# Kernel optimization log

Hardware: AMD Instinct MI355X
Metric: run time of the kernel (lower is better)

## Reference

```python
import jax, jax.numpy as jnp
import numpy as np

N_NODES = 100000
N_EDGES = 1600000
N_FEAT = 64
HIDDEN = 64
N_GRAPHS = 64
N_CLASSES = 2


def setup_inputs() -> dict:
    key = jax.random.key(0)
    ks = jax.random.split(key, 12)
    x = jax.random.normal(ks[0], (N_NODES, N_FEAT), dtype=jnp.float32)
    edge_index = jax.random.randint(ks[1], (2, N_EDGES), 0, N_NODES, dtype=jnp.int32)
    batch = jnp.sort(jax.random.randint(ks[2], (N_NODES,), 0, N_GRAPHS, dtype=jnp.int32))
    # Glorot-style init for GCNConv weights, zeros for biases (PyG default)
    def glorot(k, fan_in, fan_out):
        s = jnp.sqrt(6.0 / (fan_in + fan_out))
        return jax.random.uniform(k, (fan_in, fan_out), jnp.float32, -s, s)
    W1 = glorot(ks[3], N_FEAT, HIDDEN); b1 = jnp.zeros((HIDDEN,), jnp.float32)
    W2 = glorot(ks[4], HIDDEN, HIDDEN); b2 = jnp.zeros((HIDDEN,), jnp.float32)
    W3 = glorot(ks[5], HIDDEN, HIDDEN); b3 = jnp.zeros((HIDDEN,), jnp.float32)
    Wl = glorot(ks[6], HIDDEN, N_CLASSES); bl = jnp.zeros((N_CLASSES,), jnp.float32)
    return {"x": x, "edge_index": edge_index, "batch": batch,
            "W1": W1, "b1": b1, "W2": W2, "b2": b2, "W3": W3, "b3": b3,
            "Wl": Wl, "bl": bl}


def _gcn_conv(h, W, b, src, dst, dinv, n_nodes):
    # GCNConv with self-loops: out_i = sum_j d_i^-1/2 d_j^-1/2 (x_j W) + d_i^-1 (x_i W) + b
    h = h @ W                                   # [N, H]
    coef = (dinv[src] * dinv[dst])[:, None]     # [E, 1]
    agg = jax.ops.segment_sum(coef * h[src], dst, num_segments=n_nodes)
    return agg + (dinv * dinv)[:, None] * h + b


def reference(x, edge_index, batch, W1, b1, W2, b2, W3, b3, Wl, bl):
    src, dst = edge_index[0], edge_index[1]
    # degree of A + I (edge weight 1), shared by all three convs
    deg = jax.ops.segment_sum(jnp.ones((N_EDGES,), x.dtype), dst, num_segments=N_NODES) + 1.0
    dinv = jax.lax.rsqrt(deg)

    h = jax.nn.relu(_gcn_conv(x, W1, b1, src, dst, dinv, N_NODES))
    h = jax.nn.relu(_gcn_conv(h, W2, b2, src, dst, dinv, N_NODES))
    h = _gcn_conv(h, W3, b3, src, dst, dinv, N_NODES)

    # global_mean_pool over graph ids
    sums = jax.ops.segment_sum(h, batch, num_segments=N_GRAPHS)
    cnts = jax.ops.segment_sum(jnp.ones((N_NODES,), x.dtype), batch, num_segments=N_GRAPHS)
    pooled = sums / jnp.maximum(cnts, 1.0)[:, None]

    # dropout(p=0.5) is identity in eval mode
    return pooled @ Wl + bl
```

## Files before the change

### kernel.cpp

```cpp
#include <hip/hip_runtime.h>


#define NF 64
#define ELLW 64
#define BINSHIFT 9
#define BINW 512
#define NB 196
#define BINCAP 9216
#define LPITCH 68

typedef __attribute__((ext_vector_type(8))) _Float16 f16x8;
typedef __attribute__((ext_vector_type(4))) _Float16 f16x4;
typedef __attribute__((ext_vector_type(4))) float f32x4;

__device__ inline unsigned short f2h_u(float f) {
    return __builtin_bit_cast(unsigned short, (_Float16)f);
}
__device__ inline unsigned int pack_h2(float a, float b) {
    unsigned int ua = f2h_u(a), ub = f2h_u(b);
    return ua | (ub << 16);
}

__global__ void binA_kernel(const int* __restrict__ src, const int* __restrict__ dst,
                            int* __restrict__ binCnt, int* __restrict__ binEdges,
                            int nE, int chunk) {
    __shared__ int hist[NB];
    __shared__ int base[NB];
    int t = threadIdx.x;
    if (t < NB) hist[t] = 0;
    __syncthreads();
    int e0 = blockIdx.x * chunk;
    int e1 = min(e0 + chunk, nE);
    for (int e = e0 + t; e < e1; e += blockDim.x) {
        int b = dst[e] >> BINSHIFT;
        atomicAdd(&hist[b], 1);
    }
    __syncthreads();
    if (t < NB) {
        base[t] = atomicAdd(&binCnt[t], hist[t]);
        hist[t] = 0;
    }
    __syncthreads();
    for (int e = e0 + t; e < e1; e += blockDim.x) {
        int d = dst[e];
        int b = d >> BINSHIFT;
        int pos = base[b] + atomicAdd(&hist[b], 1);
        if (pos < BINCAP)
            binEdges[(size_t)b * BINCAP + pos] = src[e] | ((d & (BINW - 1)) << 17);
    }
}

__global__ void __launch_bounds__(512) binB_kernel(const int* __restrict__ binEdges,
                            const int* __restrict__ binCnt, int* __restrict__ cnt,
                            float* __restrict__ dinv, int* __restrict__ colELL, int n,
                            unsigned int* __restrict__ dummyA, unsigned int* __restrict__ dummyB) {
    __shared__ int lcnt[BINW];
    int t = threadIdx.x;
    int b = blockIdx.x;
    if (b == 0 && t < 32) { dummyA[t] = 0u; dummyB[t] = 0u; }
    for (int i = t; i < BINW; i += blockDim.x) lcnt[i] = 1;
    __syncthreads();
    int m = binCnt[b];
    if (m > BINCAP) m = BINCAP;
    const int* be = binEdges + (size_t)b * BINCAP;
    int nbase = b << BINSHIFT;
    for (int e = t; e < m; e += blockDim.x) {
        int v = be[e];
        int s = v & 0x1FFFF;
        int dl = v >> 17;
        int pos = atomicAdd(&lcnt[dl], 1);
        if (pos < ELLW) colELL[(size_t)(nbase + dl) * ELLW + pos] = s;
    }
    __syncthreads();
    for (int i = t; i < BINW; i += blockDim.x) {
        int node = nbase + i;
        if (node < n) {
            int c = lcnt[i];
            if (c > ELLW) c = ELLW;
            colELL[(size_t)node * ELLW + 0] = node;
            int cpad = (c + 3) & ~3;
            for (int j = c; j < cpad; ++j)
                colELL[(size_t)node * ELLW + j] = n;
            if (c <= 32) {
                int4 nv; nv.x = n; nv.y = n; nv.z = n; nv.w = n;
                for (int j = cpad; j < 32; j += 4)
                    *(int4*)(colELL + (size_t)node * ELLW + j) = nv;
            }
            cnt[node] = c;
            dinv[node] = rsqrtf((float)c);
        }
    }
}

__global__ void prep_kernel(const float* __restrict__ W1, const float* __restrict__ W2,
                            const float* __restrict__ W3, unsigned short* __restrict__ w1h,
                            unsigned short* __restrict__ w2h, unsigned short* __restrict__ w3h) {
    int t = blockIdx.x * blockDim.x + threadIdx.x;
    if (t < NF * NF) {
        w1h[t] = f2h_u(W1[t]);
        w2h[t] = f2h_u(W2[t]);
        w3h[t] = f2h_u(W3[t]);
    }
}

__device__ __forceinline__ void gather_row32(
        const unsigned short* __restrict__ hB, const int* __restrict__ cr,
        const int* __restrict__ colELL, int row, int c, int es, int fq,
        float& a0, float& a1, float& a2, float& a3) {
    int s0 = cr[0 * 4 + es], s1 = cr[1 * 4 + es];
    int s2 = cr[2 * 4 + es], s3 = cr[3 * 4 + es];
    int s4 = cr[4 * 4 + es], s5 = cr[5 * 4 + es];
    int s6 = cr[6 * 4 + es], s7 = cr[7 * 4 + es];
    f16x4 h0 = __builtin_bit_cast(f16x4, *(const uint2*)(hB + (size_t)s0 * NF + fq * 4));
    f16x4 h1 = __builtin_bit_cast(f16x4, *(const uint2*)(hB + (size_t)s1 * NF + fq * 4));
    f16x4 h2 = __builtin_bit_cast(f16x4, *(const uint2*)(hB + (size_t)s2 * NF + fq * 4));
    f16x4 h3 = __builtin_bit_cast(f16x4, *(const uint2*)(hB + (size_t)s3 * NF + fq * 4));
    f16x4 h4 = __builtin_bit_cast(f16x4, *(const uint2*)(hB + (size_t)s4 * NF + fq * 4));
    f16x4 h5 = __builtin_bit_cast(f16x4, *(const uint2*)(hB + (size_t)s5 * NF + fq * 4));
    f16x4 h6 = __builtin_bit_cast(f16x4, *(const uint2*)(hB + (size_t)s6 * NF + fq * 4));
    f16x4 h7 = __builtin_bit_cast(f16x4, *(const uint2*)(hB + (size_t)s7 * NF + fq * 4));
    f16x4 t0 = (h0 + h1) + (h2 + h3);
    f16x4 t1 = (h4 + h5) + (h6 + h7);
    a0 = (float)t0[0] + (float)t1[0];
    a1 = (float)t0[1] + (float)t1[1];
    a2 = (float)t0[2] + (float)t1[2];
    a3 = (float)t0[3] + (float)t1[3];
    if (c > 32) {
        int nq = (c + 3) >> 2;
        const int* crg = colELL + (size_t)row * ELLW;
        for (int qq = 8; qq < nq; ++qq) {
            int sg = crg[qq * 4 + es];
            f16x4 hg = __builtin_bit_cast(f16x4, *(const uint2*)(hB + (size_t)sg * NF + fq * 4));
            a0 += (float)hg[0]; a1 += (float)hg[1];
            a2 += (float)hg[2]; a3 += (float)hg[3];
        }
    }
}

__device__ inline void load_W_frags(const unsigned short* __restrict__ Wh, int r16, int kq,
                                    f16x8 bfr[4][2]) {
#pragma unroll
    for (int nt = 0; nt < 4; ++nt)
#pragma unroll
        for (int kh = 0; kh < 2; ++kh) {
            f16x8 f;
#pragma unroll
            for (int j = 0; j < 8; ++j)
                f[j] = __builtin_bit_cast(_Float16,
                        Wh[(kh * 32 + kq * 8 + j) * NF + nt * 16 + r16]);
            bfr[nt][kh] = f;
        }
}

__global__ void __launch_bounds__(256) gemm1_mfma_kernel(const float* __restrict__ A,
                                                         const unsigned short* __restrict__ Wh,
                                                         const float* __restrict__ dinv,
                                                         unsigned short* __restrict__ outB, int n) {
    __shared__ unsigned short T[4][16 * LPITCH];
    int lane = threadIdx.x & 63;
    int r16 = lane & 15, kq = lane >> 4;
    int wv = threadIdx.x >> 6;
    int wid = blockIdx.x * 4 + wv;
    int nw = gridDim.x * 4;
    f16x8 bfr[4][2];
    load_W_frags(Wh, r16, kq, bfr);
    int ntiles = n >> 4;
    for (int t = wid; t < ntiles; t += nw) {
        int r0 = t << 4;
        const float* ar = A + (size_t)(r0 + r16) * NF + kq * 8;
        f16x8 a0, a1;
        float4 v0 = *(const float4*)(ar);
        float4 v1 = *(const float4*)(ar + 4);
        float4 v2 = *(const float4*)(ar + 32);
        float4 v3 = *(const float4*)(ar + 36);
        a0[0] = (_Float16)v0.x; a0[1] = (_Float16)v0.y;
        a0[2] = (_Float16)v0.z; a0[3] = (_Float16)v0.w;
        a0[4] = (_Float16)v1.x; a0[5] = (_Float16)v1.y;
        a0[6] = (_Float16)v1.z; a0[7] = (_Float16)v1.w;
        a1[0] = (_Float16)v2.x; a1[1] = (_Float16)v2.y;
        a1[2] = (_Float16)v2.z; a1[3] = (_Float16)v2.w;
        a1[4] = (_Float16)v3.x; a1[5] = (_Float16)v3.y;
        a1[6] = (_Float16)v3.z; a1[7] = (_Float16)v3.w;
        f32x4 acc[4];
#pragma unroll
        for (int nt = 0; nt < 4; ++nt) {
            acc[nt] = (f32x4)(0.0f);
            acc[nt] = __builtin_amdgcn_mfma_f32_16x16x32_f16(a0, bfr[nt][0], acc[nt], 0, 0, 0);
            acc[nt] = __builtin_amdgcn_mfma_f32_16x16x32_f16(a1, bfr[nt][1], acc[nt], 0, 0, 0);
        }
        float ds[4];
#pragma unroll
        for (int reg = 0; reg < 4; ++reg) ds[reg] = dinv[r0 + kq * 4 + reg];
        unsigned short* Tw = T[wv];
#pragma unroll
        for (int nt = 0; nt < 4; ++nt)
#pragma unroll
            for (int reg = 0; reg < 4; ++reg)
                Tw[(kq * 4 + reg) * LPITCH + nt * 16 + r16] = f2h_u(acc[nt][reg] * ds[reg]);
#pragma unroll
        for (int it = 0; it < 4; ++it) {
            int row = it * 4 + kq;
            uint2 v = *(const uint2*)&Tw[row * LPITCH + r16 * 4];
            *(uint2*)(outB + (size_t)(r0 + row) * NF + r16 * 4) = v;
        }
    }
}

__global__ void __launch_bounds__(256) fused_agg_gemm_kernel(
        const unsigned short* __restrict__ hB, const int* __restrict__ colELL,
        const int* __restrict__ cnt, const float* __restrict__ dinv,
        const float* __restrict__ bias, const unsigned short* __restrict__ Wh,
        unsigned short* __restrict__ outB, int n) {
    __shared__ int Icol[16 * 32];
    __shared__ int Icnt[16];
    __shared__ unsigned short Tin[2048];
    __shared__ unsigned short Tout[16 * LPITCH];
    int lane = threadIdx.x & 63;
    int wv = threadIdx.x >> 6;
    int es = lane >> 4, fq = lane & 15;
    int r16 = lane & 15, kq = lane >> 4;
    int r0 = blockIdx.x << 4;
    if (threadIdx.x < 128) {
        int srow = threadIdx.x >> 3, sj = threadIdx.x & 7;
        ((int4*)Icol)[srow * 8 + sj] =
            *(const int4*)(colELL + (size_t)(r0 + srow) * ELLW + sj * 4);
    } else if (threadIdx.x < 144) {
        Icnt[threadIdx.x - 128] = cnt[r0 + threadIdx.x - 128];
    }
    f16x8 bfr0, bfr1;
    {
        f16x8 f0, f1;
#pragma unroll
        for (int j = 0; j < 8; ++j) {
            f0[j] = __builtin_bit_cast(_Float16, Wh[(kq * 8 + j) * NF + wv * 16 + r16]);
            f1[j] = __builtin_bit_cast(_Float16, Wh[(32 + kq * 8 + j) * NF + wv * 16 + r16]);
        }
        bfr0 = f0; bfr1 = f1;
    }
    __syncthreads();
#pragma unroll
    for (int rr = 0; rr < 4; ++rr) {
        int lrow = wv * 4 + rr;
        int row = r0 + lrow;
        int c = Icnt[lrow];
        const int* cr = Icol + lrow * 32;
        float a0, a1, a2, a3;
        gather_row32(hB, cr, colELL, row, c, es, fq, a0, a1, a2, a3);
        a0 += __shfl_xor(a0, 16); a1 += __shfl_xor(a1, 16);
        a2 += __shfl_xor(a2, 16); a3 += __shfl_xor(a3, 16);
        a0 += __shfl_xor(a0, 32); a1 += __shfl_xor(a1, 32);
        a2 += __shfl_xor(a2, 32); a3 += __shfl_xor(a3, 32);
        if (es == 0) {
            float dd = dinv[row];
            float4 b4 = *(const float4*)(bias + fq * 4);
            a0 = fmaxf(dd * a0 + b4.x, 0.f); a1 = fmaxf(dd * a1 + b4.y, 0.f);
            a2 = fmaxf(dd * a2 + b4.z, 0.f); a3 = fmaxf(dd * a3 + b4.w, 0.f);
            uint2 v;
            v.x = pack_h2(a0, a1);
            v.y = pack_h2(a2, a3);
            int ibase = ((fq >> 3) << 10) + (((fq >> 1) & 3) << 7)
                      + (wv * 4 + rr) * 8 + ((fq & 1) << 2);
            *(uint2*)&Tin[ibase] = v;
        }
    }
    __syncthreads();
    f16x8 A0 = *(const f16x8*)&Tin[lane * 8];
    f16x8 A1 = *(const f16x8*)&Tin[1024 + lane * 8];
    f32x4 acc = (f32x4)(0.0f);
    acc = __builtin_amdgcn_mfma_f32_16x16x32_f16(A0, bfr0, acc, 0, 0, 0);
    acc = __builtin_amdgcn_mfma_f32_16x16x32_f16(A1, bfr1, acc, 0, 0, 0);
    float ds[4];
#pragma unroll
    for (int reg = 0; reg < 4; ++reg) ds[reg] = dinv[r0 + kq * 4 + reg];
#pragma unroll
    for (int reg = 0; reg < 4; ++reg)
        Tout[(kq * 4 + reg) * LPITCH + wv * 16 + r16] = f2h_u(acc[reg] * ds[reg]);
    __syncthreads();
    int t = threadIdx.x;
    int orow = t >> 4, ocq = t & 15;
    uint2 v = *(const uint2*)&Tout[orow * LPITCH + ocq * 4];
    *(uint2*)(outB + (size_t)(r0 + orow) * NF + ocq * 4) = v;
}

__global__ void __launch_bounds__(256) gather3_pool_kernel(
        const unsigned short* __restrict__ hB, const int* __restrict__ colELL,
        const int* __restrict__ cnt, const float* __restrict__ dinv,
        const float* __restrict__ bias, const int* __restrict__ batch,
        float* __restrict__ pooled, int n) {
    __shared__ int Icol[16 * 32];
    __shared__ int Icnt[16];
    __shared__ float PL[3][NF];
    int lane = threadIdx.x & 63;
    int wv = threadIdx.x >> 6;
    int es = lane >> 4, fq = lane & 15;
    int ntiles = n >> 4;
    int first = (int)(blockIdx.x << 6);
    if (first > n - 1) first = n - 1;
    int gb = batch[first];
    if (threadIdx.x < 192) PL[threadIdx.x >> 6][threadIdx.x & 63] = 0.f;
    float4 b4 = *(const float4*)(bias + fq * 4);
#pragma unroll 1
    for (int ti = 0; ti < 4; ++ti) {
        int tile = (int)(blockIdx.x << 2) + ti;
        int r0 = tile << 4;
        bool valid = tile < ntiles;
        if (valid) {
            if (threadIdx.x < 128) {
                int srow = threadIdx.x >> 3, sj = threadIdx.x & 7;
                ((int4*)Icol)[srow * 8 + sj] =
                    *(const int4*)(colELL + (size_t)(r0 + srow) * ELLW + sj * 4);
            } else if (threadIdx.x < 144) {
                Icnt[threadIdx.x - 128] = cnt[r0 + threadIdx.x - 128];
            }
        }
        __syncthreads();
        if (valid) {
#pragma unroll
            for (int rr = 0; rr < 4; ++rr) {
                int lrow = wv * 4 + rr;
                int row = r0 + lrow;
                int c = Icnt[lrow];
                const int* cr = Icol + lrow * 32;
                float a0, a1, a2, a3;
                gather_row32(hB, cr, colELL, row, c, es, fq, a0, a1, a2, a3);
                a0 += __shfl_xor(a0, 16); a1 += __shfl_xor(a1, 16);
                a2 += __shfl_xor(a2, 16); a3 += __shfl_xor(a3, 16);
                a0 += __shfl_xor(a0, 32); a1 += __shfl_xor(a1, 32);
                a2 += __shfl_xor(a2, 32); a3 += __shfl_xor(a3, 32);
                if (es == 0) {
                    float dd = dinv[row];
                    float r0f = dd * a0 + b4.x, r1f = dd * a1 + b4.y;
                    float r2f = dd * a2 + b4.z, r3f = dd * a3 + b4.w;
                    int g = batch[row];
                    int sel = g - gb;
                    if (sel < 3) {
                        atomicAdd(&PL[sel][fq * 4 + 0], r0f);
                        atomicAdd(&PL[sel][fq * 4 + 1], r1f);
                        atomicAdd(&PL[sel][fq * 4 + 2], r2f);
                        atomicAdd(&PL[sel][fq * 4 + 3], r3f);
                    } else {
                        atomicAdd(&pooled[g * NF + fq * 4 + 0], r0f);
                        atomicAdd(&pooled[g * NF + fq * 4 + 1], r1f);
                        atomicAdd(&pooled[g * NF + fq * 4 + 2], r2f);
                        atomicAdd(&pooled[g * NF + fq * 4 + 3], r3f);
                    }
                }
            }
        }
        __syncthreads();
    }
    if (threadIdx.x < 192) {
        int s = threadIdx.x >> 6, f = threadIdx.x & 63;
        float v = PL[s][f];
        if (v != 0.f) atomicAdd(&pooled[(gb + s) * NF + f], v);
    }
}

__global__ void counts_kernel(const int* __restrict__ batch, float* __restrict__ counts, int n) {
    __shared__ int h[64];
    int t = threadIdx.x;
    if (t < 64) h[t] = 0;
    __syncthreads();
    for (int i = blockIdx.x * blockDim.x + t; i < n; i += gridDim.x * blockDim.x)
        atomicAdd(&h[batch[i]], 1);
    __syncthreads();
    if (t < 64 && h[t] > 0) atomicAdd(&counts[t], (float)h[t]);
}

__global__ void final_kernel(const float* __restrict__ pooled, const float* __restrict__ counts,
                             const float* __restrict__ Wl, const float* __restrict__ bl,
                             float* __restrict__ out) {
    int t = threadIdx.x;
    int g = t >> 1, c = t & 1;
    float inv = 1.0f / fmaxf(counts[g], 1.0f);
    float s = 0.0f;
#pragma unroll
    for (int j = 0; j < NF; ++j) s += pooled[g * NF + j] * Wl[j * 2 + c];
    out[t] = s * inv + bl[c];
}

extern "C" void kernel_launch(void* const* d_in, const int* in_sizes, int n_in,
                              void* d_out, int out_size, void* d_ws, size_t ws_size,
                              hipStream_t stream) {
    const float* x     = (const float*)d_in[0];
    const int*   ei    = (const int*)d_in[1];
    const int*   batch = (const int*)d_in[2];
    const float* W1    = (const float*)d_in[3];
    const float* b1    = (const float*)d_in[4];
    const float* W2    = (const float*)d_in[5];
    const float* b2    = (const float*)d_in[6];
    const float* W3    = (const float*)d_in[7];
    const float* b3    = (const float*)d_in[8];
    const float* Wl    = (const float*)d_in[9];
    const float* bl    = (const float*)d_in[10];
    float* out = (float*)d_out;

    const int n  = in_sizes[0] / NF;
    const int nE = in_sizes[1] / 2;
    const int* src = ei;
    const int* dst = ei + nE;

    char* ws = (char*)d_ws;
    auto alloc = [&](size_t bytes) {
        char* p = ws;
        ws += (bytes + 255) & ~(size_t)255;
        return p;
    };
    unsigned short* bufA = (unsigned short*)alloc((size_t)(n + 16) * NF * 2);
    unsigned short* bufB = (unsigned short*)alloc((size_t)(n + 16) * NF * 2);
    float* scratch = (float*)alloc((size_t)n * NF * 4);
    int*   binEdges = (int*)scratch;
    int*   colELL = (int*)alloc((size_t)n * ELLW * 4);
    float* dinv   = (float*)alloc((size_t)(n + 16) * 4);
    int*   cnt    = (int*)alloc((size_t)n * 4);
    unsigned short* w1h = (unsigned short*)alloc((size_t)NF * NF * 2);
    unsigned short* w2h = (unsigned short*)alloc((size_t)NF * NF * 2);
    unsigned short* w3h = (unsigned short*)alloc((size_t)NF * NF * 2);
    char*  ztail  = ws;
    int*   binCnt = (int*)alloc(NB * 4);
    float* pooled = (float*)alloc(64 * NF * 4);
    float* counts = (float*)alloc(64 * 4);
    size_t zbytes = (size_t)(ws - ztail);

    (void)hipMemsetAsync(ztail, 0, zbytes, stream);

    const int chunk = 3200;
    binA_kernel<<<(nE + chunk - 1) / chunk, 256, 0, stream>>>(src, dst, binCnt, binEdges, nE, chunk);
    binB_kernel<<<NB, 512, 0, stream>>>(binEdges, binCnt, cnt, dinv, colELL, n,
                                        (unsigned int*)(bufA + (size_t)n * NF),
                                        (unsigned int*)(bufB + (size_t)n * NF));
    counts_kernel<<<98, 1024, 0, stream>>>(batch, counts, n);
    prep_kernel<<<16, 256, 0, stream>>>(W1, W2, W3, w1h, w2h, w3h);

    const int tile_grid = n >> 4;

    gemm1_mfma_kernel<<<1563, 256, 0, stream>>>(x, w1h, dinv, bufA, n);
    fused_agg_gemm_kernel<<<tile_grid, 256, 0, stream>>>(bufA, colELL, cnt, dinv, b1, w2h, bufB, n);
    fused_agg_gemm_kernel<<<tile_grid, 256, 0, stream>>>(bufB, colELL, cnt, dinv, b2, w3h, bufA, n);
    gather3_pool_kernel<<<(tile_grid + 3) >> 2, 256, 0, stream>>>(bufA, colELL, cnt, dinv, b3,
                                                                  batch, pooled, n);

    final_kernel<<<1, 128, 0, stream>>>(pooled, counts, Wl, bl, out);
}
```

Before: 281.1 us.

## Gather only real ELL neighbors with interleaved rows; one tile per pool block

Drops the fixed 8-quad padded gather, which loaded padding entries pointing at a dummy row. The new loop runs only up to each row's actual neighbor quad count and interleaves the four rows per wave so their loads can be in flight together, and the padding fill in binB is removed. The pooling kernel now processes one 16-row tile per block instead of four, with a two-slot shared accumulator and more blocks. The cost is a per-row predicated, non-fixed-trip loop and more global atomics from the larger number of pool blocks.

Result: slower. 304.4 us (+8.3%).

```diff
diff --git a/kernel.cpp b/kernel.cpp
--- a/kernel.cpp
+++ b/kernel.cpp
@@ -81,11 +81,6 @@
             int cpad = (c + 3) & ~3;
             for (int j = c; j < cpad; ++j)
                 colELL[(size_t)node * ELLW + j] = n;
-            if (c <= 32) {
-                int4 nv; nv.x = n; nv.y = n; nv.z = n; nv.w = n;
-                for (int j = cpad; j < 32; j += 4)
-                    *(int4*)(colELL + (size_t)node * ELLW + j) = nv;
-            }
             cnt[node] = c;
             dinv[node] = rsqrtf((float)c);
         }
@@ -100,40 +95,6 @@
         w1h[t] = f2h_u(W1[t]);
         w2h[t] = f2h_u(W2[t]);
         w3h[t] = f2h_u(W3[t]);
-    }
-}
-
-__device__ __forceinline__ void gather_row32(
-        const unsigned short* __restrict__ hB, const int* __restrict__ cr,
-        const int* __restrict__ colELL, int row, int c, int es, int fq,
-        float& a0, float& a1, float& a2, float& a3) {
-    int s0 = cr[0 * 4 + es], s1 = cr[1 * 4 + es];
-    int s2 = cr[2 * 4 + es], s3 = cr[3 * 4 + es];
-    int s4 = cr[4 * 4 + es], s5 = cr[5 * 4 + es];
-    int s6 = cr[6 * 4 + es], s7 = cr[7 * 4 + es];
-    f16x4 h0 = __builtin_bit_cast(f16x4, *(const uint2*)(hB + (size_t)s0 * NF + fq * 4));
-    f16x4 h1 = __builtin_bit_cast(f16x4, *(const uint2*)(hB + (size_t)s1 * NF + fq * 4));
-    f16x4 h2 = __builtin_bit_cast(f16x4, *(const uint2*)(hB + (size_t)s2 * NF + fq * 4));
-    f16x4 h3 = __builtin_bit_cast(f16x4, *(const uint2*)(hB + (size_t)s3 * NF + fq * 4));
-    f16x4 h4 = __builtin_bit_cast(f16x4, *(const uint2*)(hB + (size_t)s4 * NF + fq * 4));
-    f16x4 h5 = __builtin_bit_cast(f16x4, *(const uint2*)(hB + (size_t)s5 * NF + fq * 4));
-    f16x4 h6 = __builtin_bit_cast(f16x4, *(const uint2*)(hB + (size_t)s6 * NF + fq * 4));
-    f16x4 h7 = __builtin_bit_cast(f16x4, *(const uint2*)(hB + (size_t)s7 * NF + fq * 4));
-    f16x4 t0 = (h0 + h1) + (h2 + h3);
-    f16x4 t1 = (h4 + h5) + (h6 + h7);
-    a0 = (float)t0[0] + (float)t1[0];
-    a1 = (float)t0[1] + (float)t1[1];
-    a2 = (float)t0[2] + (float)t1[2];
-    a3 = (float)t0[3] + (float)t1[3];
-    if (c > 32) {
-        int nq = (c + 3) >> 2;
-        const int* crg = colELL + (size_t)row * ELLW;
-        for (int qq = 8; qq < nq; ++qq) {
-            int sg = crg[qq * 4 + es];
-            f16x4 hg = __builtin_bit_cast(f16x4, *(const uint2*)(hB + (size_t)sg * NF + fq * 4));
-            a0 += (float)hg[0]; a1 += (float)hg[1];
-            a2 += (float)hg[2]; a3 += (float)hg[3];
-        }
     }
 }
 
@@ -238,14 +199,51 @@
         bfr0 = f0; bfr1 = f1;
     }
     __syncthreads();
+    int nqr[4]; const int* crp[4];
+    float ac[4][4];
 #pragma unroll
     for (int rr = 0; rr < 4; ++rr) {
         int lrow = wv * 4 + rr;
-        int row = r0 + lrow;
         int c = Icnt[lrow];
-        const int* cr = Icol + lrow * 32;
-        float a0, a1, a2, a3;
-        gather_row32(hB, cr, colELL, row, c, es, fq, a0, a1, a2, a3);
+        int cl = c < 32 ? c : 32;
+        nqr[rr] = (cl + 3) >> 2;
+        crp[rr] = Icol + lrow * 32;
+#pragma unroll
+        for (int k = 0; k < 4; ++k) ac[rr][k] = 0.f;
+    }
+    int nqmax = max(max(nqr[0], nqr[1]), max(nqr[2], nqr[3]));
+    for (int q = 0; q < nqmax; ++q) {
+#pragma unroll
+        for (int rr = 0; rr < 4; ++rr) {
+            if (q < nqr[rr]) {
+                int s = crp[rr][q * 4 + es];
+                f16x4 h = __builtin_bit_cast(f16x4,
+                        *(const uint2*)(hB + (size_t)s * NF + fq * 4));
+                ac[rr][0] += (float)h[0]; ac[rr][1] += (float)h[1];
+                ac[rr][2] += (float)h[2]; ac[rr][3] += (float)h[3];
+            }
+        }
+    }
+#pragma unroll
+    for (int rr = 0; rr < 4; ++rr) {
+        int lrow = wv * 4 + rr;
+        int c = Icnt[lrow];
+        if (c > 32) {
+            int nq = (c + 3) >> 2;
+            const int* crg = colELL + (size_t)(r0 + lrow) * ELLW;
+            for (int qq = 8; qq < nq; ++qq) {
+                int sg = crg[qq * 4 + es];
+                f16x4 hg = __builtin_bit_cast(f16x4,
+                        *(const uint2*)(hB + (size_t)sg * NF + fq * 4));
+                ac[rr][0] += (float)hg[0]; ac[rr][1] += (float)hg[1];
+                ac[rr][2] += (float)hg[2]; ac[rr][3] += (float)hg[3];
+            }
+        }
+    }
+#pragma unroll
+    for (int rr = 0; rr < 4; ++rr) {
+        int row = r0 + wv * 4 + rr;
+        float a0 = ac[rr][0], a1 = ac[rr][1], a2 = ac[rr][2], a3 = ac[rr][3];
         a0 += __shfl_xor(a0, 16); a1 += __shfl_xor(a1, 16);
         a2 += __shfl_xor(a2, 16); a3 += __shfl_xor(a3, 16);
         a0 += __shfl_xor(a0, 32); a1 += __shfl_xor(a1, 32);
@@ -289,67 +287,92 @@
         float* __restrict__ pooled, int n) {
     __shared__ int Icol[16 * 32];
     __shared__ int Icnt[16];
-    __shared__ float PL[3][NF];
+    __shared__ float PL[2][NF];
     int lane = threadIdx.x & 63;
     int wv = threadIdx.x >> 6;
     int es = lane >> 4, fq = lane & 15;
-    int ntiles = n >> 4;
-    int first = (int)(blockIdx.x << 6);
-    if (first > n - 1) first = n - 1;
-    int gb = batch[first];
-    if (threadIdx.x < 192) PL[threadIdx.x >> 6][threadIdx.x & 63] = 0.f;
+    int r0 = blockIdx.x << 4;
+    if (threadIdx.x < 128) {
+        int srow = threadIdx.x >> 3, sj = threadIdx.x & 7;
+        ((int4*)Icol)[srow * 8 + sj] =
+            *(const int4*)(colELL + (size_t)(r0 + srow) * ELLW + sj * 4);
+        PL[threadIdx.x >> 6][threadIdx.x & 63] = 0.f;
+    } else if (threadIdx.x < 144) {
+        Icnt[threadIdx.x - 128] = cnt[r0 + threadIdx.x - 128];
+    }
+    __syncthreads();
+    int gb = batch[r0];
     float4 b4 = *(const float4*)(bias + fq * 4);
-#pragma unroll 1
-    for (int ti = 0; ti < 4; ++ti) {
-        int tile = (int)(blockIdx.x << 2) + ti;
-        int r0 = tile << 4;
-        bool valid = tile < ntiles;
-        if (valid) {
-            if (threadIdx.x < 128) {
-                int srow = threadIdx.x >> 3, sj = threadIdx.x & 7;
-                ((int4*)Icol)[srow * 8 + sj] =
-                    *(const int4*)(colELL + (size_t)(r0 + srow) * ELLW + sj * 4);
-            } else if (threadIdx.x < 144) {
-                Icnt[threadIdx.x - 128] = cnt[r0 + threadIdx.x - 128];
+    int nqr[4]; const int* crp[4];
+    float ac[4][4];
+#pragma unroll
+    for (int rr = 0; rr < 4; ++rr) {
+        int lrow = wv * 4 + rr;
+        int c = Icnt[lrow];
+        int cl = c < 32 ? c : 32;
+        nqr[rr] = (cl + 3) >> 2;
+        crp[rr] = Icol + lrow * 32;
+#pragma unroll
+        for (int k = 0; k < 4; ++k) ac[rr][k] = 0.f;
+    }
+    int nqmax = max(max(nqr[0], nqr[1]), max(nqr[2], nqr[3]));
+    for (int q = 0; q < nqmax; ++q) {
+#pragma unroll
+        for (int rr = 0; rr < 4; ++rr) {
+            if (q < nqr[rr]) {
+                int s = crp[rr][q * 4 + es];
+                f16x4 h = __builtin_bit_cast(f16x4,
+                        *(const uint2*)(hB + (size_t)s * NF + fq * 4));
+                ac[rr][0] += (float)h[0]; ac[rr][1] += (float)h[1];
+                ac[rr][2] += (float)h[2]; ac[rr][3] += (float)h[3];
             }
         }
-        __syncthreads();
-        if (valid) {
-#pragma unroll
-            for (int rr = 0; rr < 4; ++rr) {
-                int lrow = wv * 4 + rr;
-                int row = r0 + lrow;
-                int c = Icnt[lrow];
-                const int* cr = Icol + lrow * 32;
-                float a0, a1, a2, a3;
-                gather_row32(hB, cr, colELL, row, c, es, fq, a0, a1, a2, a3);
-                a0 += __shfl_xor(a0, 16); a1 += __shfl_xor(a1, 16);
-                a2 += __shfl_xor(a2, 16); a3 += __shfl_xor(a3, 16);
-                a0 += __shfl_xor(a0, 32); a1 += __shfl_xor(a1, 32);
-                a2 += __shfl_xor(a2, 32); a3 += __shfl_xor(a3, 32);
-                if (es == 0) {
-                    float dd = dinv[row];
-                    float r0f = dd * a0 + b4.x, r1f = dd * a1 + b4.y;
-                    float r2f = dd * a2 + b4.z, r3f = dd * a3 + b4.w;
-                    int g = batch[row];
-                    int sel = g - gb;
-                    if (sel < 3) {
-                        atomicAdd(&PL[sel][fq * 4 + 0], r0f);
-                        atomicAdd(&PL[sel][fq * 4 + 1], r1f);
-                        atomicAdd(&PL[sel][fq * 4 + 2], r2f);
-                        atomicAdd(&PL[sel][fq * 4 + 3], r3f);
-                    } else {
-                        atomicAdd(&pooled[g * NF + fq * 4 + 0], r0f);
-                        atomicAdd(&pooled[g * NF + fq * 4 + 1], r1f);
-                        atomicAdd(&pooled[g * NF + fq * 4 + 2], r2f);
-                        atomicAdd(&pooled[g * NF + fq * 4 + 3], r3f);
-                    }
-                }
+    }
+#pragma unroll
+    for (int rr = 0; rr < 4; ++rr) {
+        int lrow = wv * 4 + rr;
+        int c = Icnt[lrow];
+        if (c > 32) {
+            int nq = (c + 3) >> 2;
+            const int* crg = colELL + (size_t)(r0 + lrow) * ELLW;
+            for (int qq = 8; qq < nq; ++qq) {
+                int sg = crg[qq * 4 + es];
+                f16x4 hg = __builtin_bit_cast(f16x4,
+                        *(const uint2*)(hB + (size_t)sg * NF + fq * 4));
+                ac[rr][0] += (float)hg[0]; ac[rr][1] += (float)hg[1];
+                ac[rr][2] += (float)hg[2]; ac[rr][3] += (float)hg[3];
             }
         }
-        __syncthreads();
-    }
-    if (threadIdx.x < 192) {
+    }
+#pragma unroll
+    for (int rr = 0; rr < 4; ++rr) {
+        int row = r0 + wv * 4 + rr;
+        float a0 = ac[rr][0], a1 = ac[rr][1], a2 = ac[rr][2], a3 = ac[rr][3];
+        a0 += __shfl_xor(a0, 16); a1 += __shfl_xor(a1, 16);
+        a2 += __shfl_xor(a2, 16); a3 += __shfl_xor(a3, 16);
+        a0 += __shfl_xor(a0, 32); a1 += __shfl_xor(a1, 32);
+        a2 += __shfl_xor(a2, 32); a3 += __shfl_xor(a3, 32);
+        if (es == 0) {
+            float dd = dinv[row];
+            float r0f = dd * a0 + b4.x, r1f = dd * a1 + b4.y;
+            float r2f = dd * a2 + b4.z, r3f = dd * a3 + b4.w;
+            int g = batch[row];
+            int sel = g - gb;
+            if (sel < 2) {
+                atomicAdd(&PL[sel][fq * 4 + 0], r0f);
+                atomicAdd(&PL[sel][fq * 4 + 1], r1f);
+                atomicAdd(&PL[sel][fq * 4 + 2], r2f);
+                atomicAdd(&PL[sel][fq * 4 + 3], r3f);
+            } else {
+                atomicAdd(&pooled[g * NF + fq * 4 + 0], r0f);
+                atomicAdd(&pooled[g * NF + fq * 4 + 1], r1f);
+                atomicAdd(&pooled[g * NF + fq * 4 + 2], r2f);
+                atomicAdd(&pooled[g * NF + fq * 4 + 3], r3f);
+            }
+        }
+    }
+    __syncthreads();
+    if (threadIdx.x < 128) {
         int s = threadIdx.x >> 6, f = threadIdx.x & 63;
         float v = PL[s][f];
         if (v != 0.f) atomicAdd(&pooled[(gb + s) * NF + f], v);
@@ -437,8 +460,8 @@
     gemm1_mfma_kernel<<<1563, 256, 0, stream>>>(x, w1h, dinv, bufA, n);
     fused_agg_gemm_kernel<<<tile_grid, 256, 0, stream>>>(bufA, colELL, cnt, dinv, b1, w2h, bufB, n);
     fused_agg_gemm_kernel<<<tile_grid, 256, 0, stream>>>(bufB, colELL, cnt, dinv, b2, w3h, bufA, n);
-    gather3_pool_kernel<<<(tile_grid + 3) >> 2, 256, 0, stream>>>(bufA, colELL, cnt, dinv, b3,
-                                                                  batch, pooled, n);
+    gather3_pool_kernel<<<tile_grid, 256, 0, stream>>>(bufA, colELL, cnt, dinv, b3,
+                                                       batch, pooled, n);
 
     final_kernel<<<1, 128, 0, stream>>>(pooled, counts, Wl, bl, out);
 }
```
